# Kernel tuning notes

Hardware: AMD Instinct MI355X
Metric: run time of the kernel (lower is better)

Reference implementation:

```python
import jax, jax.numpy as jnp
import numpy as np

BS, N, F_IN, H, F_OUT = 4, 2048, 128, 4, 64


def setup_inputs() -> dict:
    key = jax.random.key(0)
    k1, k2, k3, k4, k5 = jax.random.split(key, 5)
    x = jax.random.normal(k1, (BS, N, F_IN), dtype=jnp.float32)
    adj = jax.random.randint(k2, (BS, N, N), 0, 2).astype(bool)
    # guarantee self-loops so no softmax row is all -inf
    adj = jnp.logical_or(adj, jnp.eye(N, dtype=bool)[None])
    # xavier-uniform-ish scales
    w = jax.random.uniform(k3, (H, F_IN, F_OUT), dtype=jnp.float32,
                           minval=-1.0, maxval=1.0) * np.sqrt(6.0 / (F_IN + F_OUT))
    a_src = jax.random.uniform(k4, (H, F_OUT, 1), dtype=jnp.float32,
                               minval=-1.0, maxval=1.0) * np.sqrt(6.0 / (F_OUT + 1))
    a_dst = jax.random.uniform(k5, (H, F_OUT, 1), dtype=jnp.float32,
                               minval=-1.0, maxval=1.0) * np.sqrt(6.0 / (F_OUT + 1))
    bias = jnp.zeros((F_OUT,), dtype=jnp.float32)
    return {"x": x, "adj": adj, "w": w, "a_src": a_src, "a_dst": a_dst, "bias": bias}


def reference(x, adj, w, a_src, a_dst, bias):
    bs, n = x.shape[:2]
    # h_prime: [bs, H, n, F_OUT]
    h = jnp.einsum('bnf,hfo->bhno', x, w)
    th = jnp.tanh(h)
    s_src = jnp.einsum('bhno,ho->bhn', th, a_src[..., 0])  # [bs,H,n]
    s_dst = jnp.einsum('bhno,ho->bhn', th, a_dst[..., 0])  # [bs,H,n]
    # attn[b,h,i,j] = src[b,h,i] + dst[b,h,j]
    attn = s_src[..., :, None] + s_dst[..., None, :]
    attn = jnp.where(attn >= 0, attn, 0.2 * attn)  # leaky_relu(0.2)
    attn = jnp.where(adj[:, None], attn, -jnp.inf)  # mask = ~adj
    p = jax.nn.softmax(attn, axis=-1)  # dropout is identity at eval
    out = jnp.einsum('bhij,bhjo->bhio', p, h) + bias  # [bs,H,n,F_OUT]
    # torch .view(bs, n, -1) on contiguous [bs,H,n,F_OUT]: raw reshape
    return out.reshape(bs, n, -1)
```

## Files before the change

kernel.cpp:

```cpp
#include <hip/hip_runtime.h>
#include <hip/hip_fp16.h>

#define NN   2048
#define FIN  128
#define FOUT 64
#define LOG2E 1.44269504088896f

using f16x8 = __attribute__((ext_vector_type(8))) _Float16;
using f16x4 = __attribute__((ext_vector_type(4))) _Float16;
using f16x2 = __attribute__((ext_vector_type(2))) _Float16;
using f32x4 = __attribute__((ext_vector_type(4))) float;
using i32x4 = __attribute__((ext_vector_type(4))) int;

__device__ inline float fast_exp2(float x) {
#if __has_builtin(__builtin_amdgcn_exp2f)
    return __builtin_amdgcn_exp2f(x);
#else
    return exp2f(x);
#endif
}


__global__ __launch_bounds__(256) void k1_proj(
    const float* __restrict__ x, const float* __restrict__ w,
    const float* __restrict__ a_src, const float* __restrict__ a_dst,
    const int* __restrict__ adj,
    _Float16* __restrict__ h16B, float* __restrict__ ssrc, float* __restrict__ sdst,
    unsigned int* __restrict__ adjbits)
{
    __shared__ __align__(16) float w_s[FIN * FOUT];
    __shared__ __align__(16) float xs[64 * 132];

    const int t    = threadIdx.x;
    const int bx   = blockIdx.x;
    const int bh   = bx >> 5;
    const int tile = bx & 31;
    const int b    = bh >> 2;
    const int h    = bh & 3;
    const int n0   = tile * 64;

    {
        const f32x4* wg = (const f32x4*)(w + h * FIN * FOUT);
        f32x4* wl = (f32x4*)w_s;
#pragma unroll
        for (int k = 0; k < 8; ++k) wl[t + 256 * k] = wg[t + 256 * k];
    }
    {
#pragma unroll
        for (int k = 0; k < 8; ++k) {
            int q  = t + 256 * k;
            int r  = q >> 5;
            int c4 = q & 31;
            f32x4 v = *(const f32x4*)(x + (size_t)(b * NN + n0 + r) * FIN + c4 * 4);
            *(f32x4*)(xs + r * 132 + c4 * 4) = v;
        }
    }
    __syncthreads();

    const int ty = t >> 4, tx = t & 15;
    float acc[4][4] = {};

#pragma unroll 4
    for (int f4 = 0; f4 < 32; ++f4) {
        f32x4 xv[4], wv[4];
#pragma unroll
        for (int q = 0; q < 4; ++q)
            xv[q] = *(const f32x4*)(xs + (ty * 4 + q) * 132 + f4 * 4);
#pragma unroll
        for (int k = 0; k < 4; ++k)
            wv[k] = *(const f32x4*)(w_s + (f4 * 4 + k) * 64 + tx * 4);
#pragma unroll
        for (int q = 0; q < 4; ++q)
#pragma unroll
            for (int k = 0; k < 4; ++k)
#pragma unroll
                for (int c = 0; c < 4; ++c)
                    acc[q][c] += xv[q][k] * wv[k][c];
    }

    const int j0 = n0 + ty * 4;
#pragma unroll
    for (int cc = 0; cc < 4; ++cc) {
        int o = tx * 4 + cc;
        f16x4 hv;
#pragma unroll
        for (int q = 0; q < 4; ++q) hv[q] = (_Float16)acc[q][cc];
        int off = bh * 131072 + (j0 >> 5) * 2048 + (o >> 4) * 512
                + (((j0 >> 3) & 3) * 16 + (o & 15)) * 8 + (j0 & 7);
        *(f16x4*)(h16B + off) = hv;
    }

    f32x4 a_s = *(const f32x4*)(a_src + h * FOUT + tx * 4);
    f32x4 a_d = *(const f32x4*)(a_dst + h * FOUT + tx * 4);
    float ss[4], sd[4];
#pragma unroll
    for (int q = 0; q < 4; ++q) {
        float s1 = 0.f, s2 = 0.f;
#pragma unroll
        for (int cc = 0; cc < 4; ++cc) {
            float th = tanhf(acc[q][cc]);
            s1 += th * a_s[cc];
            s2 += th * a_d[cc];
        }
        ss[q] = s1; sd[q] = s2;
    }
#pragma unroll
    for (int m = 1; m <= 8; m <<= 1) {
#pragma unroll
        for (int q = 0; q < 4; ++q) {
            ss[q] += __shfl_xor(ss[q], m);
            sd[q] += __shfl_xor(sd[q], m);
        }
    }
    if (tx == 0) {
#pragma unroll
        for (int q = 0; q < 4; ++q) {
            ssrc[bh * NN + j0 + q] = ss[q] * LOG2E;
            sdst[bh * NN + j0 + q] = sd[q] * LOG2E;
        }
    }

    {
        const int  frow0 = bx * 16;
        const int* asrc  = adj + (size_t)frow0 * NN;
#pragma unroll
        for (int w4 = 0; w4 < 4; ++w4) {
            int widx  = t + 256 * w4;
            int row_l = widx >> 6;
            int wc    = widx & 63;
            const i32x4* p = (const i32x4*)(asrc + (size_t)row_l * NN + wc * 32);
            unsigned int wbits = 0;
#pragma unroll
            for (int k = 0; k < 8; ++k) {
                i32x4 v = p[k];
                wbits |= (unsigned int)(v[0] & 1) << (4 * k);
                wbits |= (unsigned int)(v[1] & 1) << (4 * k + 1);
                wbits |= (unsigned int)(v[2] & 1) << (4 * k + 2);
                wbits |= (unsigned int)(v[3] & 1) << (4 * k + 3);
            }
            adjbits[(size_t)(frow0 + row_l) * 64 + wc] = wbits;
        }
    }
}

__global__ __launch_bounds__(512, 6) void k2_attn(
    const unsigned int* __restrict__ adjbits,
    const _Float16* __restrict__ h16B,
    const float* __restrict__ ssrc, const float* __restrict__ sdst,
    const float* __restrict__ bias, float* __restrict__ out)
{
    __shared__ __align__(16) char smem[50240];
    _Float16*     Bf     = (_Float16*)smem;
    unsigned int* adjw   = (unsigned int*)(smem + 16384);
    float*        E1f    = (float*)(smem + 33792);
    float*        E2f    = (float*)(smem + 41984);
    float*        redmax = (float*)(smem + 50176);
    float*        comb   = (float*)smem;

    const int t    = threadIdx.x;
    const int wv   = t >> 6;
    const int lane = t & 63;
    const int bh   = blockIdx.x >> 5;
    const int i0   = (blockIdx.x & 31) << 6;
    const int b    = bh >> 2;
    const int rg   = wv >> 1;
    const int par  = wv & 1;
    const int m    = lane & 15;
    const int g    = lane >> 4;

    const _Float16* Bsrc = h16B + bh * 131072;

#define STAGE(bufi_, s_)                                                        \
    __builtin_amdgcn_global_load_lds(                                           \
        (const __attribute__((address_space(1))) unsigned int*)(Bsrc + (s_) * 4096 + t * 8), \
        (__attribute__((address_space(3))) unsigned int*)(Bf + (bufi_) * 4096 + t * 8), \
        16, 0, 0)

    STAGE(0, 0);

    {
        const uint4* asrc = (const uint4*)(adjbits + ((size_t)b * NN + i0) * 64);
#pragma unroll
        for (int k = 0; k < 2; ++k) {
            int idx = t + 512 * k;
            uint4 v = asrc[idx];
            unsigned int* dst = adjw + (idx >> 4) * 68 + (idx & 15) * 4;
            *(uint4*)dst = v;
        }
    }
    float dm;
    {
        f32x4 dv = *(const f32x4*)(sdst + bh * NN + t * 4);
        f32x4 e1v, e2v;
#pragma unroll
        for (int e = 0; e < 4; ++e) {
            e1v[e] = fast_exp2(dv[e]);
            e2v[e] = fast_exp2(0.2f * dv[e]);
        }
        *(f32x4*)(E1f + t * 4) = e1v;
        *(f32x4*)(E2f + t * 4) = e2v;
        dm = fmaxf(fmaxf(dv[0], dv[1]), fmaxf(dv[2], dv[3]));
#pragma unroll
        for (int msk = 1; msk <= 32; msk <<= 1) dm = fmaxf(dm, __shfl_xor(dm, msk));
        if (lane == 0) redmax[wv] = dm;
    }
    asm volatile("s_waitcnt vmcnt(0)" ::: "memory");
    __syncthreads();

    float D = redmax[0];
#pragma unroll
    for (int k = 1; k < 8; ++k) D = fmaxf(D, redmax[k]);

    const int row = i0 + rg * 16 + m;
    const float sA = ssrc[bh * NN + row];
    float c = sA + D; c = fmaxf(c, 0.2f * c);
    const float K1 = fast_exp2(sA - c);
    const float K2 = fast_exp2(fmaf(0.2f, sA, -c));

    f32x4 acc0 = {0,0,0,0}, acc1 = {0,0,0,0}, acc2 = {0,0,0,0}, acc3 = {0,0,0,0};
    f32x4 accz = {0,0,0,0};
    f16x8 ones;
#pragma unroll
    for (int i = 0; i < 8; ++i) ones[i] = (_Float16)1.0f;

    const int arow68 = (rg * 16 + m) * 68;

    for (int s = 0; s < 32; ++s) {
        if (s < 31) {
            STAGE((s + 1) & 1, s + 1);
            asm volatile("s_waitcnt vmcnt(1)" ::: "memory");
        } else {
            asm volatile("s_waitcnt vmcnt(0)" ::: "memory");
        }
        __builtin_amdgcn_sched_barrier(0);
        __builtin_amdgcn_s_barrier();
        __builtin_amdgcn_sched_barrier(0);

        const int ci = 2 * s + par;
        unsigned int wb = adjw[arow68 + ci] >> (8 * g);
        const float* e1p = E1f + ci * 32 + 8 * g;
        const float* e2p = E2f + ci * 32 + 8 * g;
        f32x4 e1a = *(const f32x4*)(e1p);
        f32x4 e1b = *(const f32x4*)(e1p + 4);
        f32x4 e2a = *(const f32x4*)(e2p);
        f32x4 e2b = *(const f32x4*)(e2p + 4);

        const _Float16* bb = Bf + (s & 1) * 4096 + par * 2048 + lane * 8;
        f16x8 b0 = *(const f16x8*)(bb);
        f16x8 b1 = *(const f16x8*)(bb + 512);
        f16x8 b2 = *(const f16x8*)(bb + 1024);
        f16x8 b3 = *(const f16x8*)(bb + 1536);

        float ev[8];
#pragma unroll
        for (int i = 0; i < 8; ++i) {
            float E1v = (i < 4) ? e1a[i] : e1b[i - 4];
            float E2v = (i < 4) ? e2a[i] : e2b[i - 4];
            float ee  = fmaxf(K1 * E1v, K2 * E2v);
            ev[i] = (wb & (1u << i)) ? ee : 0.0f;
        }
        union { f16x8 v; f16x2 p[4]; } af;
#pragma unroll
        for (int i = 0; i < 4; ++i)
            af.p[i] = __builtin_bit_cast(f16x2,
                __builtin_amdgcn_cvt_pkrtz(ev[2 * i], ev[2 * i + 1]));

        acc0 = __builtin_amdgcn_mfma_f32_16x16x32_f16(af.v, b0, acc0, 0, 0, 0);
        acc1 = __builtin_amdgcn_mfma_f32_16x16x32_f16(af.v, b1, acc1, 0, 0, 0);
        acc2 = __builtin_amdgcn_mfma_f32_16x16x32_f16(af.v, b2, acc2, 0, 0, 0);
        acc3 = __builtin_amdgcn_mfma_f32_16x16x32_f16(af.v, b3, acc3, 0, 0, 0);
        accz = __builtin_amdgcn_mfma_f32_16x16x32_f16(af.v, ones, accz, 0, 0, 0);

        __builtin_amdgcn_s_barrier();
    }
#undef STAGE

    __syncthreads();
    if (par == 1) {
        float* cp = comb + (rg * 64 + lane) * 20;
#pragma unroll
        for (int r = 0; r < 4; ++r) {
            cp[0 + r]  = acc0[r];
            cp[4 + r]  = acc1[r];
            cp[8 + r]  = acc2[r];
            cp[12 + r] = acc3[r];
            cp[16 + r] = accz[r];
        }
    }
    __syncthreads();
    if (par == 0) {
        const float* cp = comb + (rg * 64 + lane) * 20;
        float zs[4];
#pragma unroll
        for (int r = 0; r < 4; ++r) zs[r] = accz[r] + cp[16 + r];
        size_t obase = ((size_t)bh * NN + i0 + rg * 16) * FOUT;
#pragma unroll
        for (int ot = 0; ot < 4; ++ot) {
            float bv = bias[ot * 16 + m];
            f32x4 a = (ot == 0) ? acc0 : (ot == 1) ? acc1 : (ot == 2) ? acc2 : acc3;
#pragma unroll
            for (int r = 0; r < 4; ++r) {
                float v = (a[r] + cp[ot * 4 + r]) / zs[r] + bv;
                out[obase + (size_t)(g * 4 + r) * FOUT + ot * 16 + m] = v;
            }
        }
    }
}

extern "C" void kernel_launch(void* const* d_in, const int* in_sizes, int n_in,
                              void* d_out, int out_size, void* d_ws, size_t ws_size,
                              hipStream_t stream) {
    (void)in_sizes; (void)n_in; (void)out_size; (void)ws_size;
    const float* x     = (const float*)d_in[0];
    const int*   adj   = (const int*)d_in[1];
    const float* w     = (const float*)d_in[2];
    const float* a_src = (const float*)d_in[3];
    const float* a_dst = (const float*)d_in[4];
    const float* bias  = (const float*)d_in[5];
    float*       out   = (float*)d_out;

    _Float16*     h16B    = (_Float16*)d_ws;
    float*        ssrc    = (float*)((char*)d_ws + 4194304);
    float*        sdst    = (float*)((char*)d_ws + 4194304 + 131072);
    unsigned int* adjbits = (unsigned int*)((char*)d_ws + 4718592);

    k1_proj<<<512, 256, 0, stream>>>(x, w, a_src, a_dst, adj, h16B, ssrc, sdst, adjbits);
    k2_attn<<<512, 512, 0, stream>>>(adjbits, h16B, ssrc, sdst, bias, out);
}
```

Baseline: 50.58 us.

## Halve attention block to 256 threads, two row groups per wave, recompute exp per pair

The attention kernel now runs 256 threads per block, and each wave handles two 16-row groups. This reuses the B fragments loaded from LDS across twice as many MFMAs. The per-column exp tables E1/E2 are dropped. Instead, raw s_dst is staged into LDS through global_load_lds and exp2 of the leaky-relu logit is computed per element. This trades fewer LDS reads and smaller shared memory for more transcendental work and higher register pressure with ten accumulators, under a 3-blocks-per-CU launch bound.

```diff
diff --git a/kernel.cpp b/kernel.cpp
--- a/kernel.cpp
+++ b/kernel.cpp
@@ -143,18 +143,17 @@
     }
 }
 
-__global__ __launch_bounds__(512, 6) void k2_attn(
+__global__ __launch_bounds__(256, 3) void k2_attn(
     const unsigned int* __restrict__ adjbits,
     const _Float16* __restrict__ h16B,
     const float* __restrict__ ssrc, const float* __restrict__ sdst,
     const float* __restrict__ bias, float* __restrict__ out)
 {
-    __shared__ __align__(16) char smem[50240];
+    __shared__ __align__(16) char smem[42000];
     _Float16*     Bf     = (_Float16*)smem;
     unsigned int* adjw   = (unsigned int*)(smem + 16384);
-    float*        E1f    = (float*)(smem + 33792);
-    float*        E2f    = (float*)(smem + 41984);
-    float*        redmax = (float*)(smem + 50176);
+    float*        sd_lds = (float*)(smem + 33792);
+    float*        redmax = (float*)(smem + 41984);
     float*        comb   = (float*)smem;
 
     const int t    = threadIdx.x;
@@ -163,72 +162,82 @@
     const int bh   = blockIdx.x >> 5;
     const int i0   = (blockIdx.x & 31) << 6;
     const int b    = bh >> 2;
-    const int rg   = wv >> 1;
+    const int rgp  = wv >> 1;
     const int par  = wv & 1;
     const int m    = lane & 15;
     const int g    = lane >> 4;
+    const int rga  = rgp * 2;
+    const int rgb  = rgp * 2 + 1;
 
     const _Float16* Bsrc = h16B + bh * 131072;
 
-#define STAGE(bufi_, s_)                                                        \
+#define STAGE(bufi_, s_) do {                                                   \
     __builtin_amdgcn_global_load_lds(                                           \
         (const __attribute__((address_space(1))) unsigned int*)(Bsrc + (s_) * 4096 + t * 8), \
         (__attribute__((address_space(3))) unsigned int*)(Bf + (bufi_) * 4096 + t * 8), \
-        16, 0, 0)
+        16, 0, 0);                                                              \
+    __builtin_amdgcn_global_load_lds(                                           \
+        (const __attribute__((address_space(1))) unsigned int*)(Bsrc + (s_) * 4096 + 2048 + t * 8), \
+        (__attribute__((address_space(3))) unsigned int*)(Bf + (bufi_) * 4096 + 2048 + t * 8), \
+        16, 0, 0);                                                              \
+    } while (0)
 
     STAGE(0, 0);
-
     {
         const uint4* asrc = (const uint4*)(adjbits + ((size_t)b * NN + i0) * 64);
 #pragma unroll
-        for (int k = 0; k < 2; ++k) {
-            int idx = t + 512 * k;
+        for (int k = 0; k < 4; ++k) {
+            int idx = t + 256 * k;
             uint4 v = asrc[idx];
-            unsigned int* dst = adjw + (idx >> 4) * 68 + (idx & 15) * 4;
-            *(uint4*)dst = v;
-        }
-    }
-    float dm;
-    {
-        f32x4 dv = *(const f32x4*)(sdst + bh * NN + t * 4);
-        f32x4 e1v, e2v;
-#pragma unroll
-        for (int e = 0; e < 4; ++e) {
-            e1v[e] = fast_exp2(dv[e]);
-            e2v[e] = fast_exp2(0.2f * dv[e]);
-        }
-        *(f32x4*)(E1f + t * 4) = e1v;
-        *(f32x4*)(E2f + t * 4) = e2v;
-        dm = fmaxf(fmaxf(dv[0], dv[1]), fmaxf(dv[2], dv[3]));
+            *(uint4*)(adjw + (idx >> 4) * 68 + (idx & 15) * 4) = v;
+        }
+    }
+    __builtin_amdgcn_global_load_lds(
+        (const __attribute__((address_space(1))) unsigned int*)(sdst + bh * NN + t * 4),
+        (__attribute__((address_space(3))) unsigned int*)(sd_lds + t * 4), 16, 0, 0);
+    __builtin_amdgcn_global_load_lds(
+        (const __attribute__((address_space(1))) unsigned int*)(sdst + bh * NN + 1024 + t * 4),
+        (__attribute__((address_space(3))) unsigned int*)(sd_lds + 1024 + t * 4), 16, 0, 0);
+
+    const float sA_a = ssrc[bh * NN + i0 + rga * 16 + m];
+    const float sA_b = ssrc[bh * NN + i0 + rgb * 16 + m];
+
+    asm volatile("s_waitcnt vmcnt(0)" ::: "memory");
+    __syncthreads();
+
+    {
+        f32x4 d0 = *(const f32x4*)(sd_lds + t * 8);
+        f32x4 d1 = *(const f32x4*)(sd_lds + t * 8 + 4);
+        float dm = fmaxf(fmaxf(fmaxf(d0[0], d0[1]), fmaxf(d0[2], d0[3])),
+                         fmaxf(fmaxf(d1[0], d1[1]), fmaxf(d1[2], d1[3])));
 #pragma unroll
         for (int msk = 1; msk <= 32; msk <<= 1) dm = fmaxf(dm, __shfl_xor(dm, msk));
         if (lane == 0) redmax[wv] = dm;
     }
-    asm volatile("s_waitcnt vmcnt(0)" ::: "memory");
-    __syncthreads();
-
-    float D = redmax[0];
-#pragma unroll
-    for (int k = 1; k < 8; ++k) D = fmaxf(D, redmax[k]);
-
-    const int row = i0 + rg * 16 + m;
-    const float sA = ssrc[bh * NN + row];
-    float c = sA + D; c = fmaxf(c, 0.2f * c);
-    const float K1 = fast_exp2(sA - c);
-    const float K2 = fast_exp2(fmaf(0.2f, sA, -c));
-
-    f32x4 acc0 = {0,0,0,0}, acc1 = {0,0,0,0}, acc2 = {0,0,0,0}, acc3 = {0,0,0,0};
-    f32x4 accz = {0,0,0,0};
+    __syncthreads();
+    const float D = fmaxf(fmaxf(redmax[0], redmax[1]), fmaxf(redmax[2], redmax[3]));
+
+    float c_a = sA_a + D; c_a = fmaxf(c_a, 0.2f * c_a);
+    float c_b = sA_b + D; c_b = fmaxf(c_b, 0.2f * c_b);
+    const float sAc_a  = sA_a - c_a;
+    const float sAc2_a = fmaf(0.2f, sA_a, -c_a);
+    const float sAc_b  = sA_b - c_b;
+    const float sAc2_b = fmaf(0.2f, sA_b, -c_b);
+
+    f32x4 aA0 = {0,0,0,0}, aA1 = {0,0,0,0}, aA2 = {0,0,0,0}, aA3 = {0,0,0,0};
+    f32x4 aB0 = {0,0,0,0}, aB1 = {0,0,0,0}, aB2 = {0,0,0,0}, aB3 = {0,0,0,0};
+    f32x4 zA = {0,0,0,0}, zB = {0,0,0,0};
     f16x8 ones;
 #pragma unroll
     for (int i = 0; i < 8; ++i) ones[i] = (_Float16)1.0f;
 
-    const int arow68 = (rg * 16 + m) * 68;
+    const int arowA = (rga * 16 + m) * 68;
+    const int arowB = (rgb * 16 + m) * 68;
 
     for (int s = 0; s < 32; ++s) {
         if (s < 31) {
             STAGE((s + 1) & 1, s + 1);
-            asm volatile("s_waitcnt vmcnt(1)" ::: "memory");
+            asm volatile("s_waitcnt vmcnt(2)" ::: "memory");
         } else {
             asm volatile("s_waitcnt vmcnt(0)" ::: "memory");
         }
@@ -237,13 +246,11 @@
         __builtin_amdgcn_sched_barrier(0);
 
         const int ci = 2 * s + par;
-        unsigned int wb = adjw[arow68 + ci] >> (8 * g);
-        const float* e1p = E1f + ci * 32 + 8 * g;
-        const float* e2p = E2f + ci * 32 + 8 * g;
-        f32x4 e1a = *(const f32x4*)(e1p);
-        f32x4 e1b = *(const f32x4*)(e1p + 4);
-        f32x4 e2a = *(const f32x4*)(e2p);
-        f32x4 e2b = *(const f32x4*)(e2p + 4);
+        unsigned int wbA = adjw[arowA + ci] >> (8 * g);
+        unsigned int wbB = adjw[arowB + ci] >> (8 * g);
+        const float* djp = sd_lds + ci * 32 + 8 * g;
+        f32x4 dj0 = *(const f32x4*)(djp);
+        f32x4 dj1 = *(const f32x4*)(djp + 4);
 
         const _Float16* bb = Bf + (s & 1) * 4096 + par * 2048 + lane * 8;
         f16x8 b0 = *(const f16x8*)(bb);
@@ -251,25 +258,34 @@
         f16x8 b2 = *(const f16x8*)(bb + 1024);
         f16x8 b3 = *(const f16x8*)(bb + 1536);
 
-        float ev[8];
+        float evA[8], evB[8];
 #pragma unroll
         for (int i = 0; i < 8; ++i) {
-            float E1v = (i < 4) ? e1a[i] : e1b[i - 4];
-            float E2v = (i < 4) ? e2a[i] : e2b[i - 4];
-            float ee  = fmaxf(K1 * E1v, K2 * E2v);
-            ev[i] = (wb & (1u << i)) ? ee : 0.0f;
-        }
-        union { f16x8 v; f16x2 p[4]; } af;
-#pragma unroll
-        for (int i = 0; i < 4; ++i)
-            af.p[i] = __builtin_bit_cast(f16x2,
-                __builtin_amdgcn_cvt_pkrtz(ev[2 * i], ev[2 * i + 1]));
-
-        acc0 = __builtin_amdgcn_mfma_f32_16x16x32_f16(af.v, b0, acc0, 0, 0, 0);
-        acc1 = __builtin_amdgcn_mfma_f32_16x16x32_f16(af.v, b1, acc1, 0, 0, 0);
-        acc2 = __builtin_amdgcn_mfma_f32_16x16x32_f16(af.v, b2, acc2, 0, 0, 0);
-        acc3 = __builtin_amdgcn_mfma_f32_16x16x32_f16(af.v, b3, acc3, 0, 0, 0);
-        accz = __builtin_amdgcn_mfma_f32_16x16x32_f16(af.v, ones, accz, 0, 0, 0);
+            float dj = (i < 4) ? dj0[i] : dj1[i - 4];
+            float eA = fast_exp2(fmaxf(sAc_a + dj, fmaf(0.2f, dj, sAc2_a)));
+            float eB = fast_exp2(fmaxf(sAc_b + dj, fmaf(0.2f, dj, sAc2_b)));
+            evA[i] = (wbA & (1u << i)) ? eA : 0.0f;
+            evB[i] = (wbB & (1u << i)) ? eB : 0.0f;
+        }
+        union { f16x8 v; f16x2 p[4]; } afA, afB;
+#pragma unroll
+        for (int i = 0; i < 4; ++i) {
+            afA.p[i] = __builtin_bit_cast(f16x2,
+                __builtin_amdgcn_cvt_pkrtz(evA[2 * i], evA[2 * i + 1]));
+            afB.p[i] = __builtin_bit_cast(f16x2,
+                __builtin_amdgcn_cvt_pkrtz(evB[2 * i], evB[2 * i + 1]));
+        }
+
+        aA0 = __builtin_amdgcn_mfma_f32_16x16x32_f16(afA.v, b0, aA0, 0, 0, 0);
+        aA1 = __builtin_amdgcn_mfma_f32_16x16x32_f16(afA.v, b1, aA1, 0, 0, 0);
+        aA2 = __builtin_amdgcn_mfma_f32_16x16x32_f16(afA.v, b2, aA2, 0, 0, 0);
+        aA3 = __builtin_amdgcn_mfma_f32_16x16x32_f16(afA.v, b3, aA3, 0, 0, 0);
+        zA  = __builtin_amdgcn_mfma_f32_16x16x32_f16(afA.v, ones, zA, 0, 0, 0);
+        aB0 = __builtin_amdgcn_mfma_f32_16x16x32_f16(afB.v, b0, aB0, 0, 0, 0);
+        aB1 = __builtin_amdgcn_mfma_f32_16x16x32_f16(afB.v, b1, aB1, 0, 0, 0);
+        aB2 = __builtin_amdgcn_mfma_f32_16x16x32_f16(afB.v, b2, aB2, 0, 0, 0);
+        aB3 = __builtin_amdgcn_mfma_f32_16x16x32_f16(afB.v, b3, aB3, 0, 0, 0);
+        zB  = __builtin_amdgcn_mfma_f32_16x16x32_f16(afB.v, ones, zB, 0, 0, 0);
 
         __builtin_amdgcn_s_barrier();
     }
@@ -277,31 +293,39 @@
 
     __syncthreads();
     if (par == 1) {
-        float* cp = comb + (rg * 64 + lane) * 20;
+        float* cp = comb + (rgp * 64 + lane) * 41;
 #pragma unroll
         for (int r = 0; r < 4; ++r) {
-            cp[0 + r]  = acc0[r];
-            cp[4 + r]  = acc1[r];
-            cp[8 + r]  = acc2[r];
-            cp[12 + r] = acc3[r];
-            cp[16 + r] = accz[r];
+            cp[0 + r]  = aA0[r]; cp[4 + r]  = aA1[r];
+            cp[8 + r]  = aA2[r]; cp[12 + r] = aA3[r];
+            cp[16 + r] = zA[r];
+            cp[20 + r] = aB0[r]; cp[24 + r] = aB1[r];
+            cp[28 + r] = aB2[r]; cp[32 + r] = aB3[r];
+            cp[36 + r] = zB[r];
         }
     }
     __syncthreads();
     if (par == 0) {
-        const float* cp = comb + (rg * 64 + lane) * 20;
-        float zs[4];
-#pragma unroll
-        for (int r = 0; r < 4; ++r) zs[r] = accz[r] + cp[16 + r];
-        size_t obase = ((size_t)bh * NN + i0 + rg * 16) * FOUT;
+        const float* cp = comb + (rgp * 64 + lane) * 41;
+        float zsA[4], zsB[4];
+#pragma unroll
+        for (int r = 0; r < 4; ++r) {
+            zsA[r] = zA[r] + cp[16 + r];
+            zsB[r] = zB[r] + cp[36 + r];
+        }
+        size_t obaseA = ((size_t)bh * NN + i0 + rga * 16) * FOUT;
+        size_t obaseB = ((size_t)bh * NN + i0 + rgb * 16) * FOUT;
 #pragma unroll
         for (int ot = 0; ot < 4; ++ot) {
             float bv = bias[ot * 16 + m];
-            f32x4 a = (ot == 0) ? acc0 : (ot == 1) ? acc1 : (ot == 2) ? acc2 : acc3;
+            f32x4 aA = (ot == 0) ? aA0 : (ot == 1) ? aA1 : (ot == 2) ? aA2 : aA3;
+            f32x4 aB = (ot == 0) ? aB0 : (ot == 1) ? aB1 : (ot == 2) ? aB2 : aB3;
 #pragma unroll
             for (int r = 0; r < 4; ++r) {
-                float v = (a[r] + cp[ot * 4 + r]) / zs[r] + bv;
-                out[obase + (size_t)(g * 4 + r) * FOUT + ot * 16 + m] = v;
+                float vA = (aA[r] + cp[ot * 4 + r])      / zsA[r] + bv;
+                float vB = (aB[r] + cp[20 + ot * 4 + r]) / zsB[r] + bv;
+                out[obaseA + (size_t)(g * 4 + r) * FOUT + ot * 16 + m] = vA;
+                out[obaseB + (size_t)(g * 4 + r) * FOUT + ot * 16 + m] = vB;
             }
         }
     }
@@ -325,5 +349,5 @@
     unsigned int* adjbits = (unsigned int*)((char*)d_ws + 4718592);
 
     k1_proj<<<512, 256, 0, stream>>>(x, w, a_src, a_dst, adj, h16B, ssrc, sdst, adjbits);
-    k2_attn<<<512, 512, 0, stream>>>(adjbits, h16B, ssrc, sdst, bias, out);
+    k2_attn<<<512, 256, 0, stream>>>(adjbits, h16B, ssrc, sdst, bias, out);
 }
```

After: 55.51 us. 1.1x slower.
